# Kernel optimization log

Measured on AMD Instinct MI355X. Metric: run time of the kernel, lower is better.

Reference implementation:

```python
import jax, jax.numpy as jnp
import numpy as np

BN_EPS = 1e-5


def gcn_conv(x, src, dst, W, b, n_nodes):
    # PyG GCNConv with normalize=True, add_self_loops=True.
    loops = jnp.arange(n_nodes, dtype=src.dtype)
    src_a = jnp.concatenate([src, loops])
    dst_a = jnp.concatenate([dst, loops])
    ones = jnp.ones(src_a.shape[0], dtype=x.dtype)
    deg = jax.ops.segment_sum(ones, dst_a, num_segments=n_nodes)  # [N]
    dinv = jnp.where(deg > 0, jax.lax.rsqrt(deg), 0.0)
    norm = dinv[src_a] * dinv[dst_a]                               # [E+N]
    h = x @ W                                                      # [N, out]
    msg = h[src_a] * norm[:, None]                                 # [E+N, out]
    out = jax.ops.segment_sum(msg, dst_a, num_segments=n_nodes)    # [N, out]
    return out + b


def batch_norm(x, gamma, beta):
    mean = jnp.mean(x, axis=0)
    var = jnp.mean(jnp.square(x - mean), axis=0)  # biased, as in BN training fwd
    return gamma * (x - mean) * jax.lax.rsqrt(var + BN_EPS) + beta


def setup_inputs() -> dict:
    key = jax.random.key(0)
    ks = jax.random.split(key, 8)
    N, E, IN, HID, OUT = 50000, 800000, 128, 64, 40
    node_feat = jax.random.normal(ks[0], (N, IN), dtype=jnp.float32)
    edge_index = jax.random.randint(ks[1], (2, E), 0, N, dtype=jnp.int32)
    s1 = 1.0 / np.sqrt(IN)
    s2 = 1.0 / np.sqrt(HID)
    W1 = jax.random.uniform(ks[2], (IN, HID), jnp.float32, -s1, s1)
    b1 = jax.random.uniform(ks[3], (HID,), jnp.float32, -s1, s1)
    gamma = jnp.ones((HID,), jnp.float32)
    beta = jnp.zeros((HID,), jnp.float32)
    W2 = jax.random.uniform(ks[4], (HID, OUT), jnp.float32, -s2, s2)
    b2 = jax.random.uniform(ks[5], (OUT,), jnp.float32, -s2, s2)
    return {"node_feat": node_feat, "edge_index": edge_index,
            "W1": W1, "b1": b1, "gamma": gamma, "beta": beta,
            "W2": W2, "b2": b2}


def reference(node_feat, edge_index, W1, b1, gamma, beta, W2, b2):
    n_nodes = node_feat.shape[0]
    src, dst = edge_index[0], edge_index[1]
    x = gcn_conv(node_feat, src, dst, W1, b1, n_nodes)
    x = batch_norm(x, gamma, beta)
    x = jax.nn.relu(x)
    # dropout: identity (eval-mode / deterministic baseline)
    x = gcn_conv(x, src, dst, W2, b2, n_nodes)
    return x
```

## Files before the change

kernel.cpp:

```cpp
#include <hip/hip_runtime.h>
#include <hip/hip_fp16.h>

#define N_NODES 50000
#define N_EDGES 800000
#define IN_F    128
#define HID_F   64
#define OUT_F   40

#define EPB   4096
#define NBLK  ((N_EDGES + EPB - 1) / EPB)
#define NBK   ((N_NODES + 255) / 256)
#define CAP   6144
#define NREP  32
#define NB_MM ((N_NODES + 63) / 64)
#define NB_G1 ((N_NODES + 127) / 128)
#define NB_AG ((N_NODES + 31) / 32)

typedef _Float16 half8v __attribute__((ext_vector_type(8)));
typedef float    f32x4  __attribute__((ext_vector_type(4)));

union h8cv { uint4 u; __half h[8]; };


__global__ __launch_bounds__(512) void k_pre(const int* __restrict__ ei,
                                             int* __restrict__ blkcnt,
                                             unsigned int* __restrict__ bket,
                                             float* __restrict__ st2,
                                             const float* __restrict__ x,
                                             const float* __restrict__ W1,
                                             __half* __restrict__ h1r) {
    __shared__ uint4 smem4[3328];
    __shared__ int h[256], fill[256];
    __shared__ int wt[4];
    int t = threadIdx.x;

    if (blockIdx.x < NBLK) {
        unsigned int* staged = (unsigned int*)smem4;
        int lane = t & 63, wv = t >> 6;
        if (t < 256) h[t] = 0;
        if (blockIdx.x == 0)
            for (int i = t; i < NREP * 2 * HID_F; i += 512) st2[i] = 0.f;
        __syncthreads();
        int base = blockIdx.x * EPB;
        int nedge = N_EDGES - base; if (nedge > EPB) nedge = EPB;
#pragma unroll
        for (int it = 0; it < EPB / 512; ++it) {
            int e = base + it * 512 + t;
            if (e < N_EDGES) atomicAdd(&h[ei[N_EDGES + e] >> 8], 1);
        }
        __syncthreads();
        int v = (t < 256) ? h[t] : 0;
        int sv = v;
        if (t < 256) {
#pragma unroll
            for (int o = 1; o < 64; o <<= 1) {
                int u = __shfl_up(sv, o);
                if (lane >= o) sv += u;
            }
            if (lane == 63) wt[wv] = sv;
        }
        __syncthreads();
        if (t < 256) {
            int off = 0;
            if (wv > 0) off += wt[0];
            if (wv > 1) off += wt[1];
            if (wv > 2) off += wt[2];
            fill[t] = sv + off - v;
        }
        __syncthreads();
#pragma unroll
        for (int it = 0; it < EPB / 512; ++it) {
            int e = base + it * 512 + t;
            if (e < N_EDGES) {
                int srcv = ei[e], dstv = ei[N_EDGES + e];
                int p = atomicAdd(&fill[dstv >> 8], 1);
                staged[p] = ((unsigned int)dstv << 16) | (unsigned int)srcv;
            }
        }
        __syncthreads();
        for (int i = t; i < nedge; i += 512) bket[base + i] = staged[i];
        if (t < NBK) blkcnt[t * NBLK + blockIdx.x] = h[t];
        return;
    }

    _Float16 (*sA)[IN_F + 8] = (_Float16(*)[IN_F + 8])smem4;
    _Float16 (*sB)[IN_F + 8] = (_Float16(*)[IN_F + 8])((char*)smem4 + 34816);
    int bid = blockIdx.x - NBLK;
    int row0 = bid * 128;
    for (int i = t; i < 128 * 32; i += 512) {
        int r  = i >> 5;
        int c4 = i & 31;
        int gr = row0 + r;
        float4 v = make_float4(0.f, 0.f, 0.f, 0.f);
        if (gr < N_NODES) v = ((const float4*)x)[gr * 32 + c4];
        sA[r][c4 * 4 + 0] = (_Float16)v.x;
        sA[r][c4 * 4 + 1] = (_Float16)v.y;
        sA[r][c4 * 4 + 2] = (_Float16)v.z;
        sA[r][c4 * 4 + 3] = (_Float16)v.w;
    }
    for (int i = t; i < IN_F * HID_F; i += 512) {
        int k = i >> 6, n = i & 63;
        sB[n][k] = (_Float16)W1[i];
    }
    __syncthreads();

    int lane = t & 63, wid = t >> 6;
    int quad = lane >> 4, l15 = lane & 15;
    int m0 = wid * 16;
    half8v af[4];
#pragma unroll
    for (int ks = 0; ks < 4; ++ks)
        af[ks] = *(const half8v*)&sA[m0 + l15][ks * 32 + quad * 8];
    f32x4 acc[4];
#pragma unroll
    for (int nt = 0; nt < 4; ++nt) acc[nt] = (f32x4)(0.f);
#pragma unroll
    for (int nt = 0; nt < 4; ++nt) {
#pragma unroll
        for (int ks = 0; ks < 4; ++ks) {
            half8v bf = *(const half8v*)&sB[nt * 16 + l15][ks * 32 + quad * 8];
            acc[nt] = __builtin_amdgcn_mfma_f32_16x16x32_f16(af[ks], bf, acc[nt], 0, 0, 0);
        }
    }
    int rbase = row0 + m0 + quad * 4;
#pragma unroll
    for (int nt = 0; nt < 4; ++nt) {
        int col = nt * 16 + l15;
#pragma unroll
        for (int r = 0; r < 4; ++r) {
            int gr = rbase + r;
            if (gr < N_NODES)
                h1r[gr * HID_F + col] = __float2half(acc[nt][r]);
        }
    }
}


__global__ __launch_bounds__(512) void k_bucket(const int* __restrict__ blkcnt,
                                                const unsigned int* __restrict__ bket,
                                                int* __restrict__ rowptr,
                                                float* __restrict__ dinv,
                                                unsigned short* __restrict__ ssrc,
                                                int* __restrict__ perm) {
    __shared__ unsigned int keys[CAP];
    __shared__ unsigned short outb[CAP];
    __shared__ int colpre[256], rowcnt[256], boffs[256];
    __shared__ int cnt[256], fillb[256];
    __shared__ int wt[4], wsum[8], sbase, ssize;
    __shared__ int dbin[64], dfl[64];
    int b = blockIdx.x, t = threadIdx.x;
    int lane = t & 63, wid = t >> 6;

    int cp = 0, rc = 0;
    if (t < NBLK) {
#pragma unroll 4
        for (int bp = 0; bp < b; ++bp) cp += blkcnt[bp * NBLK + t];
        rc = blkcnt[b * NBLK + t];
    }
    if (t < 256) { colpre[t] = cp; rowcnt[t] = rc; }
    int red = cp;
#pragma unroll
    for (int o = 32; o > 0; o >>= 1) red += __shfl_down(red, o);
    if (lane == 0) wsum[wid] = red;
    int sv = rc;
    if (t < 256) {
#pragma unroll
        for (int o = 1; o < 64; o <<= 1) {
            int u = __shfl_up(sv, o);
            if (lane >= o) sv += u;
        }
        if (lane == 63) wt[wid] = sv;
    }
    __syncthreads();
    if (t == 0) {
        int s = 0;
#pragma unroll
        for (int r = 0; r < 8; ++r) s += wsum[r];
        sbase = s;
    }
    if (t < 256) {
        int off = 0;
        if (wid > 0) off += wt[0];
        if (wid > 1) off += wt[1];
        if (wid > 2) off += wt[2];
        boffs[t] = sv + off - rc;
        if (t == 255) ssize = sv + off;
    }
    __syncthreads();
    int base = sbase, size = ssize;

    for (int jj = wid; jj < NBLK; jj += 8) {
        int len = rowcnt[jj];
        int gs  = jj * EPB + colpre[jj];
        int d0  = boffs[jj];
        for (int o = lane; o < len; o += 64) keys[d0 + o] = bket[gs + o];
    }
    if (t < 256) cnt[t] = 0;
    __syncthreads();

    for (int i = t; i < size; i += 512) atomicAdd(&cnt[(keys[i] >> 16) & 255], 1);
    __syncthreads();
    int cv = (t < 256) ? cnt[t] : 0;
    int sv2 = cv;
    if (t < 256) {
#pragma unroll
        for (int o = 1; o < 64; o <<= 1) {
            int u = __shfl_up(sv2, o);
            if (lane >= o) sv2 += u;
        }
        if (lane == 63) wt[wid] = sv2;
    }
    __syncthreads();
    if (t < 256) {
        int off = 0;
        if (wid > 0) off += wt[0];
        if (wid > 1) off += wt[1];
        if (wid > 2) off += wt[2];
        int ex = sv2 + off - cv;
        fillb[t] = ex;
        int node = b * 256 + t;
        if (node < N_NODES) {
            rowptr[node] = base + ex;
            dinv[node]   = rsqrtf((float)cv + 1.0f);
        }
    }
    if (b == 0 && t == 0) rowptr[N_NODES] = N_EDGES;
    __syncthreads();

    for (int i = t; i < size; i += 512) {
        unsigned int k = keys[i];
        int p = atomicAdd(&fillb[(k >> 16) & 255], 1);
        outb[p] = (unsigned short)(k & 0xFFFFu);
    }
    __syncthreads();
    for (int i = t; i < size; i += 512) ssrc[base + i] = outb[i];

    if (t < 64) dbin[t] = 0;
    __syncthreads();
    int node2 = b * 256 + t;
    int dg = 63;
    if (t < 256) {
        if (node2 < N_NODES) { dg = cv; if (dg > 62) dg = 62; }
        atomicAdd(&dbin[dg], 1);
    }
    __syncthreads();
    if (t < 64) {
        int bv = dbin[t];
        int s = bv;
#pragma unroll
        for (int o = 1; o < 64; o <<= 1) {
            int u = __shfl_up(s, o);
            if (lane >= o) s += u;
        }
        dfl[t] = s - bv;
    }
    __syncthreads();
    if (t < 256) {
        int r = atomicAdd(&dfl[dg], 1);
        perm[b * 256 + r] = node2;
    }
}


__global__ __launch_bounds__(256, 8) void k_agg1(const int* __restrict__ rowptr,
                                                 const unsigned short* __restrict__ ssrc,
                                                 const float* __restrict__ dinv,
                                                 const __half* __restrict__ h1r,
                                                 const float* __restrict__ b1,
                                                 const int* __restrict__ perm,
                                                 __half* __restrict__ agg1h,
                                                 float* __restrict__ st2) {
    __shared__ float vs[32][HID_F + 1];
    int t = threadIdx.x;
    int lane = t & 63, wid = t >> 6;
    int g = lane >> 3, i = lane & 7;
    int rloc = wid * 8 + g;
    int d = perm[blockIdx.x * 32 + rloc];
    bool valid = d < N_NODES;
    int base = 0, end = 0;
    if (valid) { base = rowptr[d]; end = rowptr[d + 1]; }
    float acc[8];
#pragma unroll
    for (int c = 0; c < 8; ++c) acc[c] = 0.f;

    for (int cc = base; cc < end; cc += 8) {
        int nrem = end - cc; if (nrem > 8) nrem = 8;
        int e = (i < nrem) ? (int)ssrc[cc + i] : 0;
#pragma unroll
        for (int kb = 0; kb < 8; kb += 4) {
            if (kb < nrem) {
                int sk[4]; uint4 v[4]; float w[4];
#pragma unroll
                for (int k = 0; k < 4; ++k)
                    sk[k] = __shfl(e, (lane & 56) + kb + k);
#pragma unroll
                for (int k = 0; k < 4; ++k) {
                    if (kb + k < nrem) {
                        v[k] = ((const uint4*)(h1r + (size_t)sk[k] * HID_F))[i];
                        w[k] = dinv[sk[k]];
                    } else { v[k] = make_uint4(0, 0, 0, 0); w[k] = 0.f; }
                }
#pragma unroll
                for (int k = 0; k < 4; ++k) {
                    h8cv cv; cv.u = v[k];
#pragma unroll
                    for (int c = 0; c < 8; ++c)
                        acc[c] += w[k] * __half2float(cv.h[c]);
                }
            }
        }
    }

    float val[8];
    if (valid) {
        float di = dinv[d];
        h8cv self; self.u = ((const uint4*)(h1r + (size_t)d * HID_F))[i];
        const float4 b1a = ((const float4*)b1)[i * 2];
        const float4 b1b = ((const float4*)b1)[i * 2 + 1];
        val[0] = (acc[0] + di * __half2float(self.h[0])) * di + b1a.x;
        val[1] = (acc[1] + di * __half2float(self.h[1])) * di + b1a.y;
        val[2] = (acc[2] + di * __half2float(self.h[2])) * di + b1a.z;
        val[3] = (acc[3] + di * __half2float(self.h[3])) * di + b1a.w;
        val[4] = (acc[4] + di * __half2float(self.h[4])) * di + b1b.x;
        val[5] = (acc[5] + di * __half2float(self.h[5])) * di + b1b.y;
        val[6] = (acc[6] + di * __half2float(self.h[6])) * di + b1b.z;
        val[7] = (acc[7] + di * __half2float(self.h[7])) * di + b1b.w;
        h8cv ov;
#pragma unroll
        for (int c = 0; c < 8; ++c) ov.h[c] = __float2half(val[c]);
        ((uint4*)(agg1h + (size_t)d * HID_F))[i] = ov.u;
    } else {
#pragma unroll
        for (int c = 0; c < 8; ++c) val[c] = 0.f;
    }
#pragma unroll
    for (int c = 0; c < 8; ++c) vs[rloc][i * 8 + c] = val[c];
    __syncthreads();
    if (t < HID_F) {
        float sm = 0.f, s2 = 0.f;
#pragma unroll 4
        for (int r = 0; r < 32; ++r) {
            float v2 = vs[r][t];
            sm += v2; s2 += v2 * v2;
        }
        float* strow = st2 + (blockIdx.x & (NREP - 1)) * (2 * HID_F);
        atomicAdd(&strow[t], sm);
        atomicAdd(&strow[HID_F + t], s2);
    }
}


__global__ __launch_bounds__(256) void k_gemm2(const __half* __restrict__ agg1h,
                                               const float* __restrict__ st2,
                                               const float* __restrict__ gamma,
                                               const float* __restrict__ beta,
                                               const float* __restrict__ W2,
                                               const float* __restrict__ dinv,
                                               __half* __restrict__ h2p) {
    __shared__ _Float16 sA[64][HID_F + 8];
    __shared__ _Float16 sB[48][HID_F + 8];
    __shared__ float sScale[HID_F], sShift[HID_F];
    int t = threadIdx.x;
    if (t < HID_F) {
        float sm = 0.f, s2 = 0.f;
#pragma unroll
        for (int r = 0; r < NREP; ++r) {
            sm += st2[r * (2 * HID_F) + t];
            s2 += st2[r * (2 * HID_F) + HID_F + t];
        }
        float mean = sm * (1.0f / N_NODES);
        float var  = s2 * (1.0f / N_NODES) - mean * mean;
        float inv  = rsqrtf(var + 1e-5f);
        float gv   = gamma[t];
        sScale[t]  = gv * inv;
        sShift[t]  = beta[t] - gv * inv * mean;
    }
    for (int i = t; i < 48 * HID_F; i += 256) {
        int k = i / 48, n = i - k * 48;
        sB[n][k] = (n < OUT_F) ? (_Float16)W2[k * OUT_F + n] : (_Float16)0.f;
    }
    __syncthreads();
    int row0 = blockIdx.x * 64;
    for (int i = t; i < 64 * HID_F; i += 256) {
        int r = i >> 6, k = i & 63;
        int gr = row0 + r;
        float v = 0.f;
        if (gr < N_NODES) {
            float a = __half2float(agg1h[gr * HID_F + k]);
            v = fmaxf(a * sScale[k] + sShift[k], 0.f);
        }
        sA[r][k] = (_Float16)v;
    }
    __syncthreads();

    int lane = t & 63, wid = t >> 6;
    int quad = lane >> 4, l15 = lane & 15;
    int m0 = wid * 16;
    half8v af[2];
#pragma unroll
    for (int ks = 0; ks < 2; ++ks)
        af[ks] = *(const half8v*)&sA[m0 + l15][ks * 32 + quad * 8];
    f32x4 acc[3];
#pragma unroll
    for (int nt = 0; nt < 3; ++nt) acc[nt] = (f32x4)(0.f);
#pragma unroll
    for (int nt = 0; nt < 3; ++nt) {
#pragma unroll
        for (int ks = 0; ks < 2; ++ks) {
            half8v bf = *(const half8v*)&sB[nt * 16 + l15][ks * 32 + quad * 8];
            acc[nt] = __builtin_amdgcn_mfma_f32_16x16x32_f16(af[ks], bf, acc[nt], 0, 0, 0);
        }
    }
    float dv[4];
    int rbase = row0 + m0 + quad * 4;
#pragma unroll
    for (int r = 0; r < 4; ++r)
        dv[r] = (rbase + r < N_NODES) ? dinv[rbase + r] : 0.f;
#pragma unroll
    for (int nt = 0; nt < 3; ++nt) {
        int col = nt * 16 + l15;
        if (col < OUT_F) {
#pragma unroll
            for (int r = 0; r < 4; ++r) {
                int gr = rbase + r;
                if (gr < N_NODES)
                    h2p[(size_t)gr * OUT_F + col] = __float2half(acc[nt][r] * dv[r]);
            }
        }
    }
}


__global__ __launch_bounds__(256, 8) void k_agg2(const int* __restrict__ rowptr,
                                                 const unsigned short* __restrict__ ssrc,
                                                 const float* __restrict__ dinv,
                                                 const __half* __restrict__ h2p,
                                                 const float* __restrict__ b2,
                                                 const int* __restrict__ perm,
                                                 float* __restrict__ out) {
    int t = threadIdx.x;
    int lane = t & 63, wid = t >> 6;
    int g = lane >> 3, i = lane & 7;
    int rloc = wid * 8 + g;
    int d = perm[blockIdx.x * 32 + rloc];
    bool valid = d < N_NODES;
    int base = 0, end = 0;
    if (valid) { base = rowptr[d]; end = rowptr[d + 1]; }
    float acc[8];
#pragma unroll
    for (int c = 0; c < 8; ++c) acc[c] = 0.f;

    for (int cc = base; cc < end; cc += 8) {
        int nrem = end - cc; if (nrem > 8) nrem = 8;
        int e = (i < nrem) ? (int)ssrc[cc + i] : 0;
#pragma unroll
        for (int kb = 0; kb < 8; kb += 4) {
            if (kb < nrem) {
                int sk[4];
#pragma unroll
                for (int k = 0; k < 4; ++k)
                    sk[k] = __shfl(e, (lane & 56) + kb + k);
                if (i < 5) {
                    uint4 v[4];
#pragma unroll
                    for (int k = 0; k < 4; ++k) {
                        if (kb + k < nrem)
                            v[k] = ((const uint4*)(h2p + (size_t)sk[k] * OUT_F))[i];
                        else v[k] = make_uint4(0, 0, 0, 0);
                    }
#pragma unroll
                    for (int k = 0; k < 4; ++k) {
                        h8cv cv; cv.u = v[k];
#pragma unroll
                        for (int c = 0; c < 8; ++c)
                            acc[c] += __half2float(cv.h[c]);
                    }
                }
            }
        }
    }

    if (valid && i < 5) {
        h8cv self; self.u = ((const uint4*)(h2p + (size_t)d * OUT_F))[i];
        float di = dinv[d];
        const float4 b2a = ((const float4*)b2)[i * 2];
        const float4 b2b = ((const float4*)b2)[i * 2 + 1];
        float4 o0, o1;
        o0.x = (acc[0] + __half2float(self.h[0])) * di + b2a.x;
        o0.y = (acc[1] + __half2float(self.h[1])) * di + b2a.y;
        o0.z = (acc[2] + __half2float(self.h[2])) * di + b2a.z;
        o0.w = (acc[3] + __half2float(self.h[3])) * di + b2a.w;
        o1.x = (acc[4] + __half2float(self.h[4])) * di + b2b.x;
        o1.y = (acc[5] + __half2float(self.h[5])) * di + b2b.y;
        o1.z = (acc[6] + __half2float(self.h[6])) * di + b2b.z;
        o1.w = (acc[7] + __half2float(self.h[7])) * di + b2b.w;
        float4* op = (float4*)(out + (size_t)d * OUT_F + i * 8);
        op[0] = o0;
        op[1] = o1;
    }
}


extern "C" void kernel_launch(void* const* d_in, const int* in_sizes, int n_in,
                              void* d_out, int out_size, void* d_ws, size_t ws_size,
                              hipStream_t stream) {
    const float* x     = (const float*)d_in[0];
    const int*   ei    = (const int*)d_in[1];
    const float* W1    = (const float*)d_in[2];
    const float* b1    = (const float*)d_in[3];
    const float* gamma = (const float*)d_in[4];
    const float* beta  = (const float*)d_in[5];
    const float* W2    = (const float*)d_in[6];
    const float* b2    = (const float*)d_in[7];
    float* out = (float*)d_out;

    char* ws = (char*)d_ws;
    int*            blkcnt = (int*)           (ws + 0);
    int*            rowptr = (int*)           (ws + 154624);
    float*          dinv   = (float*)         (ws + 356352);
    float*          st2    = (float*)         (ws + 558080);
    unsigned int*   bket   = (unsigned int*)  (ws + 574464);
    unsigned short* ssrc   = (unsigned short*)(ws + 3785728);
    __half*         h1r    = (__half*)        (ws + 5387264);
    __half*         agg1h  = (__half*)        (ws + 11787264);
    __half*         h2p    = (__half*)        (ws + 18187264);
    int*            perm   = (int*)           (ws + 22187264);

    k_pre<<<NBLK + NB_G1, 512, 0, stream>>>(ei, blkcnt, bket, st2, x, W1, h1r);
    k_bucket<<<NBK, 512, 0, stream>>>(blkcnt, bket, rowptr, dinv, ssrc, perm);
    k_agg1<<<NB_AG, 256, 0, stream>>>(rowptr, ssrc, dinv, h1r, b1, perm, agg1h, st2);
    k_gemm2<<<NB_MM, 256, 0, stream>>>(agg1h, st2, gamma, beta, W2, dinv, h2p);
    k_agg2<<<NB_AG, 256, 0, stream>>>(rowptr, ssrc, dinv, h2p, b2, perm, out);
}
```

Before: 168.1 us.

## Move GEMM1 into bucket kernel and precompute per-block column prefix offsets

```diff
diff --git a/kernel.cpp b/kernel.cpp
--- a/kernel.cpp
+++ b/kernel.cpp
@@ -22,70 +22,200 @@
 union h8cv { uint4 u; __half h[8]; };
 
 
-__global__ __launch_bounds__(512) void k_pre(const int* __restrict__ ei,
+__global__ __launch_bounds__(512) void k_bin(const int* __restrict__ ei,
                                              int* __restrict__ blkcnt,
+                                             int* __restrict__ colpre_g,
                                              unsigned int* __restrict__ bket,
-                                             float* __restrict__ st2,
+                                             float* __restrict__ st2) {
+    __shared__ unsigned int staged[EPB];
+    __shared__ int h[256], fill[256];
+    __shared__ int wt[4];
+    int t = threadIdx.x;
+    int lane = t & 63, wv = t >> 6;
+    if (t < 256) h[t] = 0;
+    if (blockIdx.x == 0)
+        for (int i = t; i < NREP * 2 * HID_F; i += 512) st2[i] = 0.f;
+    __syncthreads();
+    int base = blockIdx.x * EPB;
+    int nedge = N_EDGES - base; if (nedge > EPB) nedge = EPB;
+#pragma unroll
+    for (int it = 0; it < EPB / 512; ++it) {
+        int e = base + it * 512 + t;
+        if (e < N_EDGES) atomicAdd(&h[ei[N_EDGES + e] >> 8], 1);
+    }
+    __syncthreads();
+    int v = (t < 256) ? h[t] : 0;
+    int sv = v;
+    if (t < 256) {
+#pragma unroll
+        for (int o = 1; o < 64; o <<= 1) {
+            int u = __shfl_up(sv, o);
+            if (lane >= o) sv += u;
+        }
+        if (lane == 63) wt[wv] = sv;
+    }
+    __syncthreads();
+    if (t < 256) {
+        int off = 0;
+        if (wv > 0) off += wt[0];
+        if (wv > 1) off += wt[1];
+        if (wv > 2) off += wt[2];
+        int ex = sv + off - v;
+        fill[t] = ex;
+        if (t < NBK) colpre_g[t * NBLK + blockIdx.x] = ex;
+    }
+    __syncthreads();
+#pragma unroll
+    for (int it = 0; it < EPB / 512; ++it) {
+        int e = base + it * 512 + t;
+        if (e < N_EDGES) {
+            int srcv = ei[e], dstv = ei[N_EDGES + e];
+            int p = atomicAdd(&fill[dstv >> 8], 1);
+            staged[p] = ((unsigned int)dstv << 16) | (unsigned int)srcv;
+        }
+    }
+    __syncthreads();
+    for (int i = t; i < nedge; i += 512) bket[base + i] = staged[i];
+    if (t < NBK) blkcnt[t * NBLK + blockIdx.x] = h[t];
+}
+
+
+__global__ __launch_bounds__(512) void k_mid(const int* __restrict__ blkcnt,
+                                             const int* __restrict__ colpre_g,
+                                             const unsigned int* __restrict__ bket,
+                                             int* __restrict__ rowptr,
+                                             float* __restrict__ dinv,
+                                             unsigned short* __restrict__ ssrc,
+                                             int* __restrict__ perm,
                                              const float* __restrict__ x,
                                              const float* __restrict__ W1,
                                              __half* __restrict__ h1r) {
-    __shared__ uint4 smem4[3328];
-    __shared__ int h[256], fill[256];
-    __shared__ int wt[4];
+    __shared__ uint4 pool[3328];
+    __shared__ int colpre[256], rowcnt[256], boffs[256];
+    __shared__ int cnt[256], fillb[256];
+    __shared__ int wt[4], wsum[8], sbase, ssize;
+    __shared__ int dbin[64], dfl[64];
     int t = threadIdx.x;
-
-    if (blockIdx.x < NBLK) {
-        unsigned int* staged = (unsigned int*)smem4;
-        int lane = t & 63, wv = t >> 6;
-        if (t < 256) h[t] = 0;
-        if (blockIdx.x == 0)
-            for (int i = t; i < NREP * 2 * HID_F; i += 512) st2[i] = 0.f;
-        __syncthreads();
-        int base = blockIdx.x * EPB;
-        int nedge = N_EDGES - base; if (nedge > EPB) nedge = EPB;
-#pragma unroll
-        for (int it = 0; it < EPB / 512; ++it) {
-            int e = base + it * 512 + t;
-            if (e < N_EDGES) atomicAdd(&h[ei[N_EDGES + e] >> 8], 1);
-        }
-        __syncthreads();
-        int v = (t < 256) ? h[t] : 0;
-        int sv = v;
+    int lane = t & 63, wid = t >> 6;
+
+    if (blockIdx.x < NBK) {
+        unsigned int*   keys = (unsigned int*)pool;
+        unsigned short* outb = (unsigned short*)((char*)pool + 24576);
+        int b = blockIdx.x;
+
+        int cp = 0, rc = 0;
+        if (t < NBLK) {
+            cp = colpre_g[b * NBLK + t];
+            rc = blkcnt[b * NBLK + t];
+        }
+        if (t < 256) { colpre[t] = cp; rowcnt[t] = rc; }
+        int red = cp;
+#pragma unroll
+        for (int o = 32; o > 0; o >>= 1) red += __shfl_down(red, o);
+        if (lane == 0) wsum[wid] = red;
+        int sv = rc;
         if (t < 256) {
 #pragma unroll
             for (int o = 1; o < 64; o <<= 1) {
                 int u = __shfl_up(sv, o);
                 if (lane >= o) sv += u;
             }
-            if (lane == 63) wt[wv] = sv;
-        }
-        __syncthreads();
+            if (lane == 63) wt[wid] = sv;
+        }
+        __syncthreads();
+        if (t == 0) {
+            int s = 0;
+#pragma unroll
+            for (int r = 0; r < 8; ++r) s += wsum[r];
+            sbase = s;
+        }
         if (t < 256) {
             int off = 0;
-            if (wv > 0) off += wt[0];
-            if (wv > 1) off += wt[1];
-            if (wv > 2) off += wt[2];
-            fill[t] = sv + off - v;
-        }
-        __syncthreads();
-#pragma unroll
-        for (int it = 0; it < EPB / 512; ++it) {
-            int e = base + it * 512 + t;
-            if (e < N_EDGES) {
-                int srcv = ei[e], dstv = ei[N_EDGES + e];
-                int p = atomicAdd(&fill[dstv >> 8], 1);
-                staged[p] = ((unsigned int)dstv << 16) | (unsigned int)srcv;
-            }
-        }
-        __syncthreads();
-        for (int i = t; i < nedge; i += 512) bket[base + i] = staged[i];
-        if (t < NBK) blkcnt[t * NBLK + blockIdx.x] = h[t];
+            if (wid > 0) off += wt[0];
+            if (wid > 1) off += wt[1];
+            if (wid > 2) off += wt[2];
+            boffs[t] = sv + off - rc;
+            if (t == 255) ssize = sv + off;
+        }
+        __syncthreads();
+        int base = sbase, size = ssize;
+
+        for (int jj = wid; jj < NBLK; jj += 8) {
+            int len = rowcnt[jj];
+            int gs  = jj * EPB + colpre[jj];
+            int d0  = boffs[jj];
+            for (int o = lane; o < len; o += 64) keys[d0 + o] = bket[gs + o];
+        }
+        if (t < 256) cnt[t] = 0;
+        __syncthreads();
+
+        for (int i = t; i < size; i += 512) atomicAdd(&cnt[(keys[i] >> 16) & 255], 1);
+        __syncthreads();
+        int cv = (t < 256) ? cnt[t] : 0;
+        int sv2 = cv;
+        if (t < 256) {
+#pragma unroll
+            for (int o = 1; o < 64; o <<= 1) {
+                int u = __shfl_up(sv2, o);
+                if (lane >= o) sv2 += u;
+            }
+            if (lane == 63) wt[wid] = sv2;
+        }
+        __syncthreads();
+        if (t < 256) {
+            int off = 0;
+            if (wid > 0) off += wt[0];
+            if (wid > 1) off += wt[1];
+            if (wid > 2) off += wt[2];
+            int ex = sv2 + off - cv;
+            fillb[t] = ex;
+            int node = b * 256 + t;
+            if (node < N_NODES) {
+                rowptr[node] = base + ex;
+                dinv[node]   = rsqrtf((float)cv + 1.0f);
+            }
+        }
+        if (b == 0 && t == 0) rowptr[N_NODES] = N_EDGES;
+        __syncthreads();
+
+        for (int i = t; i < size; i += 512) {
+            unsigned int k = keys[i];
+            int p = atomicAdd(&fillb[(k >> 16) & 255], 1);
+            outb[p] = (unsigned short)(k & 0xFFFFu);
+        }
+        __syncthreads();
+        for (int i = t; i < size; i += 512) ssrc[base + i] = outb[i];
+
+        if (t < 64) dbin[t] = 0;
+        __syncthreads();
+        int node2 = b * 256 + t;
+        int dg = 63;
+        if (t < 256) {
+            if (node2 < N_NODES) { dg = cv; if (dg > 62) dg = 62; }
+            atomicAdd(&dbin[dg], 1);
+        }
+        __syncthreads();
+        if (t < 64) {
+            int bv = dbin[t];
+            int s = bv;
+#pragma unroll
+            for (int o = 1; o < 64; o <<= 1) {
+                int u = __shfl_up(s, o);
+                if (lane >= o) s += u;
+            }
+            dfl[t] = s - bv;
+        }
+        __syncthreads();
+        if (t < 256) {
+            int r = atomicAdd(&dfl[dg], 1);
+            perm[b * 256 + r] = node2;
+        }
         return;
     }
 
-    _Float16 (*sA)[IN_F + 8] = (_Float16(*)[IN_F + 8])smem4;
-    _Float16 (*sB)[IN_F + 8] = (_Float16(*)[IN_F + 8])((char*)smem4 + 34816);
-    int bid = blockIdx.x - NBLK;
+    _Float16 (*sA)[IN_F + 8] = (_Float16(*)[IN_F + 8])pool;
+    _Float16 (*sB)[IN_F + 8] = (_Float16(*)[IN_F + 8])((char*)pool + 34816);
+    int bid = blockIdx.x - NBK;
     int row0 = bid * 128;
     for (int i = t; i < 128 * 32; i += 512) {
         int r  = i >> 5;
@@ -104,7 +234,6 @@
     }
     __syncthreads();
 
-    int lane = t & 63, wid = t >> 6;
     int quad = lane >> 4, l15 = lane & 15;
     int m0 = wid * 16;
     half8v af[4];
@@ -132,132 +261,6 @@
             if (gr < N_NODES)
                 h1r[gr * HID_F + col] = __float2half(acc[nt][r]);
         }
-    }
-}
-
-
-__global__ __launch_bounds__(512) void k_bucket(const int* __restrict__ blkcnt,
-                                                const unsigned int* __restrict__ bket,
-                                                int* __restrict__ rowptr,
-                                                float* __restrict__ dinv,
-                                                unsigned short* __restrict__ ssrc,
-                                                int* __restrict__ perm) {
-    __shared__ unsigned int keys[CAP];
-    __shared__ unsigned short outb[CAP];
-    __shared__ int colpre[256], rowcnt[256], boffs[256];
-    __shared__ int cnt[256], fillb[256];
-    __shared__ int wt[4], wsum[8], sbase, ssize;
-    __shared__ int dbin[64], dfl[64];
-    int b = blockIdx.x, t = threadIdx.x;
-    int lane = t & 63, wid = t >> 6;
-
-    int cp = 0, rc = 0;
-    if (t < NBLK) {
-#pragma unroll 4
-        for (int bp = 0; bp < b; ++bp) cp += blkcnt[bp * NBLK + t];
-        rc = blkcnt[b * NBLK + t];
-    }
-    if (t < 256) { colpre[t] = cp; rowcnt[t] = rc; }
-    int red = cp;
-#pragma unroll
-    for (int o = 32; o > 0; o >>= 1) red += __shfl_down(red, o);
-    if (lane == 0) wsum[wid] = red;
-    int sv = rc;
-    if (t < 256) {
-#pragma unroll
-        for (int o = 1; o < 64; o <<= 1) {
-            int u = __shfl_up(sv, o);
-            if (lane >= o) sv += u;
-        }
-        if (lane == 63) wt[wid] = sv;
-    }
-    __syncthreads();
-    if (t == 0) {
-        int s = 0;
-#pragma unroll
-        for (int r = 0; r < 8; ++r) s += wsum[r];
-        sbase = s;
-    }
-    if (t < 256) {
-        int off = 0;
-        if (wid > 0) off += wt[0];
-        if (wid > 1) off += wt[1];
-        if (wid > 2) off += wt[2];
-        boffs[t] = sv + off - rc;
-        if (t == 255) ssize = sv + off;
-    }
-    __syncthreads();
-    int base = sbase, size = ssize;
-
-    for (int jj = wid; jj < NBLK; jj += 8) {
-        int len = rowcnt[jj];
-        int gs  = jj * EPB + colpre[jj];
-        int d0  = boffs[jj];
-        for (int o = lane; o < len; o += 64) keys[d0 + o] = bket[gs + o];
-    }
-    if (t < 256) cnt[t] = 0;
-    __syncthreads();
-
-    for (int i = t; i < size; i += 512) atomicAdd(&cnt[(keys[i] >> 16) & 255], 1);
-    __syncthreads();
-    int cv = (t < 256) ? cnt[t] : 0;
-    int sv2 = cv;
-    if (t < 256) {
-#pragma unroll
-        for (int o = 1; o < 64; o <<= 1) {
-            int u = __shfl_up(sv2, o);
-            if (lane >= o) sv2 += u;
-        }
-        if (lane == 63) wt[wid] = sv2;
-    }
-    __syncthreads();
-    if (t < 256) {
-        int off = 0;
-        if (wid > 0) off += wt[0];
-        if (wid > 1) off += wt[1];
-        if (wid > 2) off += wt[2];
-        int ex = sv2 + off - cv;
-        fillb[t] = ex;
-        int node = b * 256 + t;
-        if (node < N_NODES) {
-            rowptr[node] = base + ex;
-            dinv[node]   = rsqrtf((float)cv + 1.0f);
-        }
-    }
-    if (b == 0 && t == 0) rowptr[N_NODES] = N_EDGES;
-    __syncthreads();
-
-    for (int i = t; i < size; i += 512) {
-        unsigned int k = keys[i];
-        int p = atomicAdd(&fillb[(k >> 16) & 255], 1);
-        outb[p] = (unsigned short)(k & 0xFFFFu);
-    }
-    __syncthreads();
-    for (int i = t; i < size; i += 512) ssrc[base + i] = outb[i];
-
-    if (t < 64) dbin[t] = 0;
-    __syncthreads();
-    int node2 = b * 256 + t;
-    int dg = 63;
-    if (t < 256) {
-        if (node2 < N_NODES) { dg = cv; if (dg > 62) dg = 62; }
-        atomicAdd(&dbin[dg], 1);
-    }
-    __syncthreads();
-    if (t < 64) {
-        int bv = dbin[t];
-        int s = bv;
-#pragma unroll
-        for (int o = 1; o < 64; o <<= 1) {
-            int u = __shfl_up(s, o);
-            if (lane >= o) s += u;
-        }
-        dfl[t] = s - bv;
-    }
-    __syncthreads();
-    if (t < 256) {
-        int r = atomicAdd(&dfl[dg], 1);
-        perm[b * 256 + r] = node2;
     }
 }
 
@@ -525,9 +528,11 @@
     __half*         agg1h  = (__half*)        (ws + 11787264);
     __half*         h2p    = (__half*)        (ws + 18187264);
     int*            perm   = (int*)           (ws + 22187264);
-
-    k_pre<<<NBLK + NB_G1, 512, 0, stream>>>(ei, blkcnt, bket, st2, x, W1, h1r);
-    k_bucket<<<NBK, 512, 0, stream>>>(blkcnt, bket, rowptr, dinv, ssrc, perm);
+    int*            cpre   = (int*)           (ws + 22387968);
+
+    k_bin<<<NBLK, 512, 0, stream>>>(ei, blkcnt, cpre, bket, st2);
+    k_mid<<<NBK + NB_G1, 512, 0, stream>>>(blkcnt, cpre, bket, rowptr, dinv, ssrc,
+                                           perm, x, W1, h1r);
     k_agg1<<<NB_AG, 256, 0, stream>>>(rowptr, ssrc, dinv, h1r, b1, perm, agg1h, st2);
     k_gemm2<<<NB_MM, 256, 0, stream>>>(agg1h, st2, gamma, beta, W2, dinv, h2p);
     k_agg2<<<NB_AG, 256, 0, stream>>>(rowptr, ssrc, dinv, h2p, b2, perm, out);
```

Measured after the change: 158.5 us. -5.7%, faster.
